# Optimization experiments

Hardware: AMD Instinct MI355X
Metric: run time of the kernel (lower is better)

## Reference

```python
import jax, jax.numpy as jnp
import numpy as np

H = 64
EPS = 1e-5


def _lstm_layer(x, w_ih, w_hh, b_ih, b_hh):
    """Single LSTM layer, batch_first input x: [B, T, I]. PyTorch gate order i,f,g,o."""
    B, T, _ = x.shape
    # precompute input contributions for all timesteps: [B, T, 4H]
    xw = jnp.einsum('bti,gi->btg', x, w_ih) + (b_ih + b_hh)
    xw = jnp.swapaxes(xw, 0, 1)  # [T, B, 4H] for scan over time

    def step(carry, xw_t):
        h, c = carry
        gates = xw_t + h @ w_hh.T  # [B, 4H]
        i, f, g, o = jnp.split(gates, 4, axis=-1)
        i = jax.nn.sigmoid(i)
        f = jax.nn.sigmoid(f)
        g = jnp.tanh(g)
        o = jax.nn.sigmoid(o)
        c = f * c + i * g
        h = o * jnp.tanh(c)
        return (h, c), h

    h0 = jnp.zeros((B, H), x.dtype)
    (_, _), hs = jax.lax.scan(step, (h0, h0), xw)
    return jnp.swapaxes(hs, 0, 1)  # [B, T, H]


def setup_inputs() -> dict:
    key = jax.random.key(0)
    ks = jax.random.split(key, 16)
    B, T, F = 4096, 256, 32
    s = 1.0 / np.sqrt(H)  # PyTorch LSTM init scale
    inp = {
        'x': jax.random.normal(ks[0], (B, T, F), jnp.float32),
        'w_ih0': jax.random.uniform(ks[1], (4 * H, F), jnp.float32, -s, s),
        'w_hh0': jax.random.uniform(ks[2], (4 * H, H), jnp.float32, -s, s),
        'b_ih0': jax.random.uniform(ks[3], (4 * H,), jnp.float32, -s, s),
        'b_hh0': jax.random.uniform(ks[4], (4 * H,), jnp.float32, -s, s),
        'w_ih1': jax.random.uniform(ks[5], (4 * H, H), jnp.float32, -s, s),
        'w_hh1': jax.random.uniform(ks[6], (4 * H, H), jnp.float32, -s, s),
        'b_ih1': jax.random.uniform(ks[7], (4 * H,), jnp.float32, -s, s),
        'b_hh1': jax.random.uniform(ks[8], (4 * H,), jnp.float32, -s, s),
        'ln_g': jnp.ones((H,), jnp.float32),
        'ln_b': jnp.zeros((H,), jnp.float32),
        'w1': jax.random.uniform(ks[9], (64, H), jnp.float32, -s, s),
        'b1': jax.random.uniform(ks[10], (64,), jnp.float32, -s, s),
        'w2': jax.random.uniform(ks[11], (1, 64), jnp.float32, -0.125, 0.125),
        'b2': jax.random.uniform(ks[12], (1,), jnp.float32, -0.125, 0.125),
    }
    return inp


def reference(x, w_ih0, w_hh0, b_ih0, b_hh0, w_ih1, w_hh1, b_ih1, b_hh1,
              ln_g, ln_b, w1, b1, w2, b2):
    out0 = _lstm_layer(x, w_ih0, w_hh0, b_ih0, b_hh0)      # [B, T, H]
    out1 = _lstm_layer(out0, w_ih1, w_hh1, b_ih1, b_hh1)   # [B, T, H]
    last = out1[:, -1, :]                                   # [B, H]
    # LayerNorm
    mu = jnp.mean(last, axis=-1, keepdims=True)
    var = jnp.mean(jnp.square(last - mu), axis=-1, keepdims=True)
    ln = (last - mu) * jax.lax.rsqrt(var + EPS) * ln_g + ln_b
    # MLP head
    h = jax.nn.relu(ln @ w1.T + b1)
    y = h @ w2.T + b2                                       # [B, 1]
    return y[:, 0]
```

## Files before the change

kernel.cpp:

```cpp
#include <hip/hip_runtime.h>

#define TSEQ 256
#define FIN  32
#define HID  64

typedef _Float16 f16x8 __attribute__((ext_vector_type(8)));
typedef float    f32x4 __attribute__((ext_vector_type(4)));

__device__ __forceinline__ float wsum(float v) {
    #pragma unroll
    for (int off = 32; off > 0; off >>= 1) v += __shfl_xor(v, off, 64);
    return v;
}

__device__ __forceinline__ float lstm_cell(const f32x4 g, float& c) {
    float ei = __expf(-g[0]);
    float ef = __expf(-g[1]);
    float yg = __expf(2.0f * g[2]);
    float eo = __expf(-g[3]);
    float sf = __builtin_amdgcn_rcpf(1.0f + ef);
    float ig = (yg - 1.0f) * __builtin_amdgcn_rcpf((1.0f + ei) * (yg + 1.0f));
    c = fmaf(sf, c, ig);
    float cc = fminf(fmaxf(c, -15.0f), 15.0f);
    float yc = __expf(2.0f * cc);
    return (yc - 1.0f) * __builtin_amdgcn_rcpf((1.0f + eo) * (yc + 1.0f));
}

__global__ __launch_bounds__(1024, 4)
void lstm_fused(const float* __restrict__ x,
                const float* __restrict__ w_ih0, const float* __restrict__ w_hh0,
                const float* __restrict__ b_ih0, const float* __restrict__ b_hh0,
                const float* __restrict__ w_ih1, const float* __restrict__ w_hh1,
                const float* __restrict__ b_ih1, const float* __restrict__ b_hh1,
                const float* __restrict__ ln_g, const float* __restrict__ ln_b,
                const float* __restrict__ w1, const float* __restrict__ b1,
                const float* __restrict__ w2, const float* __restrict__ b2,
                float* __restrict__ out)
{
    __shared__ __align__(16) _Float16 X[2][16][32];
    __shared__ __align__(16) _Float16 H0[2][16][72];
    __shared__ __align__(16) _Float16 H1[2][16][72];
    __shared__ __align__(16) float HF[16][68];
    __shared__ __align__(16) float LNB[16][64];

    const int tid  = threadIdx.x;
    const int wave = tid >> 6;
    const int lane = tid & 63;
    const int q    = lane >> 4;
    const int lm   = lane & 15;
    const int q8   = q * 8;
    const int b0   = blockIdx.x * 16;

    const int np   = wave * 16 + lm;
    const int drow = np >> 2;
    const int ty   = np & 3;
    const int row  = ty * 64 + drow;
    const int dq   = wave * 4 + q;

    f16x8 w0f[3], w1f[4];
    f32x4 bias0, bias1;
    {
        const float* p0 = w_ih0 + row * FIN + q8;
        const float* p1 = w_hh0 + row * HID + q8;
        const float* p2 = w_hh0 + row * HID + 32 + q8;
        const float* p3 = w_ih1 + row * HID + q8;
        const float* p4 = w_ih1 + row * HID + 32 + q8;
        const float* p5 = w_hh1 + row * HID + q8;
        const float* p6 = w_hh1 + row * HID + 32 + q8;
        #pragma unroll
        for (int j = 0; j < 8; ++j) {
            w0f[0][j] = (_Float16)p0[j];
            w0f[1][j] = (_Float16)p1[j];
            w0f[2][j] = (_Float16)p2[j];
            w1f[0][j] = (_Float16)p3[j];
            w1f[1][j] = (_Float16)p4[j];
            w1f[2][j] = (_Float16)p5[j];
            w1f[3][j] = (_Float16)p6[j];
        }
        #pragma unroll
        for (int r = 0; r < 4; ++r) {
            bias0[r] = b_ih0[r * 64 + dq] + b_hh0[r * 64 + dq];
            bias1[r] = b_ih1[r * 64 + dq] + b_hh1[r * 64 + dq];
        }
    }

    for (int i = tid; i < 2 * 16 * 72; i += 1024) {
        ((_Float16*)H0)[i] = (_Float16)0.0f;
        ((_Float16*)H1)[i] = (_Float16)0.0f;
    }
    const bool xlane = lane < 32;
    const int  xcol  = lane & 31;
    const float* xbase = x + (size_t)(b0 + wave) * TSEQ * FIN + xcol;
    if (xlane) X[0][wave][xcol] = (_Float16)xbase[0];
    float xw = xbase[FIN];

    float c0 = 0.0f, c1 = 0.0f;
    __syncthreads();

#define INTERVAL(P, DO_A, DO_B, DO_XSTORE, DO_XLOAD, XI)                        \
    {                                                                           \
        float xnew = 0.0f;                                                      \
        if (DO_XLOAD) xnew = xbase[(size_t)(XI) * FIN];                         \
        f16x8 rh0a = *reinterpret_cast<const f16x8*>(&H0[(P) ^ 1][lm][q8]);     \
        f16x8 rh0b = *reinterpret_cast<const f16x8*>(&H0[(P) ^ 1][lm][32 + q8]);\
        if (DO_A) {                                                             \
            f16x8 rx = *reinterpret_cast<const f16x8*>(&X[P][lm][q8]);          \
            f32x4 aA = bias0;                                                   \
            aA = __builtin_amdgcn_mfma_f32_16x16x32_f16(w0f[0], rx,   aA, 0, 0, 0); \
            aA = __builtin_amdgcn_mfma_f32_16x16x32_f16(w0f[1], rh0a, aA, 0, 0, 0); \
            aA = __builtin_amdgcn_mfma_f32_16x16x32_f16(w0f[2], rh0b, aA, 0, 0, 0); \
            float hA = lstm_cell(aA, c0);                                       \
            H0[P][lm][dq] = (_Float16)hA;                                       \
        }                                                                       \
        if (DO_B) {                                                             \
            f16x8 rh1a = *reinterpret_cast<const f16x8*>(&H1[P][lm][q8]);       \
            f16x8 rh1b = *reinterpret_cast<const f16x8*>(&H1[P][lm][32 + q8]);  \
            f32x4 aB = bias1;                                                   \
            aB = __builtin_amdgcn_mfma_f32_16x16x32_f16(w1f[0], rh0a, aB, 0, 0, 0); \
            aB = __builtin_amdgcn_mfma_f32_16x16x32_f16(w1f[1], rh0b, aB, 0, 0, 0); \
            aB = __builtin_amdgcn_mfma_f32_16x16x32_f16(w1f[2], rh1a, aB, 0, 0, 0); \
            aB = __builtin_amdgcn_mfma_f32_16x16x32_f16(w1f[3], rh1b, aB, 0, 0, 0); \
            float hB = lstm_cell(aB, c1);                                       \
            H1[(P) ^ 1][lm][dq] = (_Float16)hB;                                 \
            lastB = hB;                                                         \
        }                                                                       \
        if (DO_XSTORE && xlane) X[(P) ^ 1][wave][xcol] = (_Float16)xw;          \
        xw = xnew;                                                              \
        __syncthreads();                                                        \
    }

    float lastB = 0.0f;

    INTERVAL(0, true, false, true, true, 2)

    #pragma unroll 1
    for (int ii = 0; ii < 127; ++ii) {
        const int i1  = 2 * ii + 1;
        const int xiA = (i1 + 2 > 255) ? 255 : i1 + 2;
        const int xiB = (i1 + 3 > 255) ? 255 : i1 + 3;
        INTERVAL(1, true, true, true, true, xiA)
        INTERVAL(0, true, true, true, true, xiB)
    }

    INTERVAL(1, true, true, false, false, 0)
    INTERVAL(0, false, true, false, false, 0)
    HF[lm][dq] = lastB;
    __syncthreads();

#undef INTERVAL

    const float lngv = ln_g[lane], lnbv = ln_b[lane];
    const float b1v = b1[lane], w2v = w2[lane];
    const float* w1row = w1 + lane * 64;
    {
        float v  = HF[wave][lane];
        float mu = wsum(v) * (1.0f / 64.0f);
        float dv = v - mu;
        float var = wsum(dv * dv) * (1.0f / 64.0f);
        float ln = dv * rsqrtf(var + 1e-5f) * lngv + lnbv;
        LNB[wave][lane] = ln;
        float s = b1v;
        #pragma unroll
        for (int dd = 0; dd < 64; ++dd)
            s = fmaf(LNB[wave][dd], w1row[dd], s);
        s = fmaxf(s, 0.0f);
        float y = wsum(s * w2v);
        if (lane == 0) out[b0 + wave] = y + b2[0];
    }
}

extern "C" void kernel_launch(void* const* d_in, const int* in_sizes, int n_in,
                              void* d_out, int out_size, void* d_ws, size_t ws_size,
                              hipStream_t stream) {
    const float* x     = (const float*)d_in[0];
    const float* w_ih0 = (const float*)d_in[1];
    const float* w_hh0 = (const float*)d_in[2];
    const float* b_ih0 = (const float*)d_in[3];
    const float* b_hh0 = (const float*)d_in[4];
    const float* w_ih1 = (const float*)d_in[5];
    const float* w_hh1 = (const float*)d_in[6];
    const float* b_ih1 = (const float*)d_in[7];
    const float* b_hh1 = (const float*)d_in[8];
    const float* ln_g  = (const float*)d_in[9];
    const float* ln_b  = (const float*)d_in[10];
    const float* w1    = (const float*)d_in[11];
    const float* b1    = (const float*)d_in[12];
    const float* w2    = (const float*)d_in[13];
    const float* b2    = (const float*)d_in[14];
    lstm_fused<<<dim3(256), dim3(1024), 0, stream>>>(
        x, w_ih0, w_hh0, b_ih0, b_hh0,
        w_ih1, w_hh1, b_ih1, b_hh1,
        ln_g, ln_b, w1, b1, w2, b2, (float*)d_out);
}
```

Measured before the change: 372.3 us.

## Specialize waves per LSTM layer and fold exp scaling into weights

Each wave now serves a single LSTM layer: waves 0-7 run layer 0 and waves 8-15 run layer 1. Each wave computes two gate tiles with interleaved independent MFMA chains, so no wave runs both layers' serial MFMA-plus-activation chain in one interval. The -log2e and 2·log2e factors are pre-multiplied into the fp16 weights and biases so the activations use exp2 directly. The x staging through shared memory is also dropped: layer-0 waves load x for the next step straight from global into registers. Trade-offs are possible load imbalance (layer-0 waves do 6 MFMAs, layer-1 waves do 8) and a small fp16 rounding change from the scaled weights.

Result: slower. 420.6 us (+13.0%).

```diff
diff --git a/kernel.cpp b/kernel.cpp
--- a/kernel.cpp
+++ b/kernel.cpp
@@ -3,6 +3,9 @@
 #define TSEQ 256
 #define FIN  32
 #define HID  64
+
+#define LOG2E    1.4426950408889634f
+#define TWOLOG2E 2.8853900817779268f
 
 typedef _Float16 f16x8 __attribute__((ext_vector_type(8)));
 typedef float    f32x4 __attribute__((ext_vector_type(4)));
@@ -14,15 +17,15 @@
 }
 
 __device__ __forceinline__ float lstm_cell(const f32x4 g, float& c) {
-    float ei = __expf(-g[0]);
-    float ef = __expf(-g[1]);
-    float yg = __expf(2.0f * g[2]);
-    float eo = __expf(-g[3]);
+    float ei = __builtin_exp2f(g[0]);
+    float ef = __builtin_exp2f(g[1]);
+    float yg = __builtin_exp2f(g[2]);
+    float eo = __builtin_exp2f(g[3]);
     float sf = __builtin_amdgcn_rcpf(1.0f + ef);
     float ig = (yg - 1.0f) * __builtin_amdgcn_rcpf((1.0f + ei) * (yg + 1.0f));
     c = fmaf(sf, c, ig);
     float cc = fminf(fmaxf(c, -15.0f), 15.0f);
-    float yc = __expf(2.0f * cc);
+    float yc = __builtin_exp2f(TWOLOG2E * cc);
     return (yc - 1.0f) * __builtin_amdgcn_rcpf((1.0f + eo) * (yc + 1.0f));
 }
 
@@ -37,7 +40,6 @@
                 const float* __restrict__ w2, const float* __restrict__ b2,
                 float* __restrict__ out)
 {
-    __shared__ __align__(16) _Float16 X[2][16][32];
     __shared__ __align__(16) _Float16 H0[2][16][72];
     __shared__ __align__(16) _Float16 H1[2][16][72];
     __shared__ __align__(16) float HF[16][68];
@@ -51,103 +53,155 @@
     const int q8   = q * 8;
     const int b0   = blockIdx.x * 16;
 
-    const int np   = wave * 16 + lm;
-    const int drow = np >> 2;
-    const int ty   = np & 3;
-    const int row  = ty * 64 + drow;
-    const int dq   = wave * 4 + q;
-
-    f16x8 w0f[3], w1f[4];
+    const bool isA = wave < 8;
+    const int  wt  = wave & 7;
+    const int  T0  = 2 * wt, T1 = T0 + 1;
+    const int  np0  = T0 * 16 + lm;
+    const int  np1  = T1 * 16 + lm;
+    const int  row0 = (np0 & 3) * 64 + (np0 >> 2);
+    const int  row1 = (np1 & 3) * 64 + (np1 >> 2);
+    const int  d0 = T0 * 4 + q;
+    const int  d1 = T1 * 4 + q;
+    const float wsc = ((lm & 3) == 2) ? TWOLOG2E : -LOG2E;
+
+    f16x8 wf[8];
     f32x4 bias0, bias1;
-    {
-        const float* p0 = w_ih0 + row * FIN + q8;
-        const float* p1 = w_hh0 + row * HID + q8;
-        const float* p2 = w_hh0 + row * HID + 32 + q8;
-        const float* p3 = w_ih1 + row * HID + q8;
-        const float* p4 = w_ih1 + row * HID + 32 + q8;
-        const float* p5 = w_hh1 + row * HID + q8;
-        const float* p6 = w_hh1 + row * HID + 32 + q8;
+    if (isA) {
+        const float* p0 = w_ih0 + row0 * FIN + q8;
+        const float* p1 = w_hh0 + row0 * HID + q8;
+        const float* p2 = w_hh0 + row0 * HID + 32 + q8;
+        const float* p3 = w_ih0 + row1 * FIN + q8;
+        const float* p4 = w_hh0 + row1 * HID + q8;
+        const float* p5 = w_hh0 + row1 * HID + 32 + q8;
         #pragma unroll
         for (int j = 0; j < 8; ++j) {
-            w0f[0][j] = (_Float16)p0[j];
-            w0f[1][j] = (_Float16)p1[j];
-            w0f[2][j] = (_Float16)p2[j];
-            w1f[0][j] = (_Float16)p3[j];
-            w1f[1][j] = (_Float16)p4[j];
-            w1f[2][j] = (_Float16)p5[j];
-            w1f[3][j] = (_Float16)p6[j];
+            wf[0][j] = (_Float16)(wsc * p0[j]);
+            wf[1][j] = (_Float16)(wsc * p1[j]);
+            wf[2][j] = (_Float16)(wsc * p2[j]);
+            wf[3][j] = (_Float16)(wsc * p3[j]);
+            wf[4][j] = (_Float16)(wsc * p4[j]);
+            wf[5][j] = (_Float16)(wsc * p5[j]);
         }
         #pragma unroll
         for (int r = 0; r < 4; ++r) {
-            bias0[r] = b_ih0[r * 64 + dq] + b_hh0[r * 64 + dq];
-            bias1[r] = b_ih1[r * 64 + dq] + b_hh1[r * 64 + dq];
-        }
+            const float s = (r == 2) ? TWOLOG2E : -LOG2E;
+            bias0[r] = s * (b_ih0[r * 64 + d0] + b_hh0[r * 64 + d0]);
+            bias1[r] = s * (b_ih0[r * 64 + d1] + b_hh0[r * 64 + d1]);
+        }
+    } else {
+        const float* p0 = w_ih1 + row0 * HID + q8;
+        const float* p1 = w_ih1 + row0 * HID + 32 + q8;
+        const float* p2 = w_hh1 + row0 * HID + q8;
+        const float* p3 = w_hh1 + row0 * HID + 32 + q8;
+        const float* p4 = w_ih1 + row1 * HID + q8;
+        const float* p5 = w_ih1 + row1 * HID + 32 + q8;
+        const float* p6 = w_hh1 + row1 * HID + q8;
+        const float* p7 = w_hh1 + row1 * HID + 32 + q8;
+        #pragma unroll
+        for (int j = 0; j < 8; ++j) {
+            wf[0][j] = (_Float16)(wsc * p0[j]);
+            wf[1][j] = (_Float16)(wsc * p1[j]);
+            wf[2][j] = (_Float16)(wsc * p2[j]);
+            wf[3][j] = (_Float16)(wsc * p3[j]);
+            wf[4][j] = (_Float16)(wsc * p4[j]);
+            wf[5][j] = (_Float16)(wsc * p5[j]);
+            wf[6][j] = (_Float16)(wsc * p6[j]);
+            wf[7][j] = (_Float16)(wsc * p7[j]);
+        }
+        #pragma unroll
+        for (int r = 0; r < 4; ++r) {
+            const float s = (r == 2) ? TWOLOG2E : -LOG2E;
+            bias0[r] = s * (b_ih1[r * 64 + d0] + b_hh1[r * 64 + d0]);
+            bias1[r] = s * (b_ih1[r * 64 + d1] + b_hh1[r * 64 + d1]);
+        }
+    }
+
+    const float* xp = x + (size_t)(b0 + lm) * TSEQ * FIN + q8;
+    f32x4 xfa, xfb;
+    if (isA) {
+        xfa = *reinterpret_cast<const f32x4*>(xp);
+        xfb = *reinterpret_cast<const f32x4*>(xp + 4);
     }
 
     for (int i = tid; i < 2 * 16 * 72; i += 1024) {
         ((_Float16*)H0)[i] = (_Float16)0.0f;
         ((_Float16*)H1)[i] = (_Float16)0.0f;
     }
-    const bool xlane = lane < 32;
-    const int  xcol  = lane & 31;
-    const float* xbase = x + (size_t)(b0 + wave) * TSEQ * FIN + xcol;
-    if (xlane) X[0][wave][xcol] = (_Float16)xbase[0];
-    float xw = xbase[FIN];
-
-    float c0 = 0.0f, c1 = 0.0f;
+    float c0a = 0.0f, c0b = 0.0f, c1a = 0.0f, c1b = 0.0f;
+    float lastB0 = 0.0f, lastB1 = 0.0f;
     __syncthreads();
 
-#define INTERVAL(P, DO_A, DO_B, DO_XSTORE, DO_XLOAD, XI)                        \
-    {                                                                           \
-        float xnew = 0.0f;                                                      \
-        if (DO_XLOAD) xnew = xbase[(size_t)(XI) * FIN];                         \
-        f16x8 rh0a = *reinterpret_cast<const f16x8*>(&H0[(P) ^ 1][lm][q8]);     \
-        f16x8 rh0b = *reinterpret_cast<const f16x8*>(&H0[(P) ^ 1][lm][32 + q8]);\
-        if (DO_A) {                                                             \
-            f16x8 rx = *reinterpret_cast<const f16x8*>(&X[P][lm][q8]);          \
-            f32x4 aA = bias0;                                                   \
-            aA = __builtin_amdgcn_mfma_f32_16x16x32_f16(w0f[0], rx,   aA, 0, 0, 0); \
-            aA = __builtin_amdgcn_mfma_f32_16x16x32_f16(w0f[1], rh0a, aA, 0, 0, 0); \
-            aA = __builtin_amdgcn_mfma_f32_16x16x32_f16(w0f[2], rh0b, aA, 0, 0, 0); \
-            float hA = lstm_cell(aA, c0);                                       \
-            H0[P][lm][dq] = (_Float16)hA;                                       \
-        }                                                                       \
-        if (DO_B) {                                                             \
-            f16x8 rh1a = *reinterpret_cast<const f16x8*>(&H1[P][lm][q8]);       \
-            f16x8 rh1b = *reinterpret_cast<const f16x8*>(&H1[P][lm][32 + q8]);  \
-            f32x4 aB = bias1;                                                   \
-            aB = __builtin_amdgcn_mfma_f32_16x16x32_f16(w1f[0], rh0a, aB, 0, 0, 0); \
-            aB = __builtin_amdgcn_mfma_f32_16x16x32_f16(w1f[1], rh0b, aB, 0, 0, 0); \
-            aB = __builtin_amdgcn_mfma_f32_16x16x32_f16(w1f[2], rh1a, aB, 0, 0, 0); \
-            aB = __builtin_amdgcn_mfma_f32_16x16x32_f16(w1f[3], rh1b, aB, 0, 0, 0); \
-            float hB = lstm_cell(aB, c1);                                       \
-            H1[(P) ^ 1][lm][dq] = (_Float16)hB;                                 \
-            lastB = hB;                                                         \
-        }                                                                       \
-        if (DO_XSTORE && xlane) X[(P) ^ 1][wave][xcol] = (_Float16)xw;          \
-        xw = xnew;                                                              \
-        __syncthreads();                                                        \
-    }
-
-    float lastB = 0.0f;
-
-    INTERVAL(0, true, false, true, true, 2)
+#define MFMA __builtin_amdgcn_mfma_f32_16x16x32_f16
+#define INTERVAL(P, DO_A, DO_B, DO_XL, XI)                                          \
+    {                                                                               \
+        if (isA) {                                                                  \
+            f16x8 xcur;                                                             \
+            xcur[0] = (_Float16)xfa[0]; xcur[1] = (_Float16)xfa[1];                 \
+            xcur[2] = (_Float16)xfa[2]; xcur[3] = (_Float16)xfa[3];                 \
+            xcur[4] = (_Float16)xfb[0]; xcur[5] = (_Float16)xfb[1];                 \
+            xcur[6] = (_Float16)xfb[2]; xcur[7] = (_Float16)xfb[3];                 \
+            if (DO_XL) {                                                            \
+                xfa = *reinterpret_cast<const f32x4*>(xp + (size_t)(XI) * FIN);     \
+                xfb = *reinterpret_cast<const f32x4*>(xp + (size_t)(XI) * FIN + 4); \
+            }                                                                       \
+            if (DO_A) {                                                             \
+                f16x8 rh0a = *reinterpret_cast<const f16x8*>(&H0[(P) ^ 1][lm][q8]);      \
+                f16x8 rh0b = *reinterpret_cast<const f16x8*>(&H0[(P) ^ 1][lm][32 + q8]); \
+                f32x4 a0 = bias0, a1 = bias1;                                       \
+                a0 = MFMA(wf[0], xcur, a0, 0, 0, 0);                                \
+                a1 = MFMA(wf[3], xcur, a1, 0, 0, 0);                                \
+                a0 = MFMA(wf[1], rh0a, a0, 0, 0, 0);                                \
+                a1 = MFMA(wf[4], rh0a, a1, 0, 0, 0);                                \
+                a0 = MFMA(wf[2], rh0b, a0, 0, 0, 0);                                \
+                a1 = MFMA(wf[5], rh0b, a1, 0, 0, 0);                                \
+                float hv0 = lstm_cell(a0, c0a);                                     \
+                float hv1 = lstm_cell(a1, c0b);                                     \
+                H0[P][lm][d0] = (_Float16)hv0;                                      \
+                H0[P][lm][d1] = (_Float16)hv1;                                      \
+            }                                                                       \
+        } else if (DO_B) {                                                          \
+            f16x8 rh0a = *reinterpret_cast<const f16x8*>(&H0[(P) ^ 1][lm][q8]);      \
+            f16x8 rh0b = *reinterpret_cast<const f16x8*>(&H0[(P) ^ 1][lm][32 + q8]); \
+            f16x8 rh1a = *reinterpret_cast<const f16x8*>(&H1[P][lm][q8]);            \
+            f16x8 rh1b = *reinterpret_cast<const f16x8*>(&H1[P][lm][32 + q8]);       \
+            f32x4 a0 = bias0, a1 = bias1;                                           \
+            a0 = MFMA(wf[0], rh0a, a0, 0, 0, 0);                                    \
+            a1 = MFMA(wf[4], rh0a, a1, 0, 0, 0);                                    \
+            a0 = MFMA(wf[1], rh0b, a0, 0, 0, 0);                                    \
+            a1 = MFMA(wf[5], rh0b, a1, 0, 0, 0);                                    \
+            a0 = MFMA(wf[2], rh1a, a0, 0, 0, 0);                                    \
+            a1 = MFMA(wf[6], rh1a, a1, 0, 0, 0);                                    \
+            a0 = MFMA(wf[3], rh1b, a0, 0, 0, 0);                                    \
+            a1 = MFMA(wf[7], rh1b, a1, 0, 0, 0);                                    \
+            float hv0 = lstm_cell(a0, c1a);                                         \
+            float hv1 = lstm_cell(a1, c1b);                                         \
+            H1[(P) ^ 1][lm][d0] = (_Float16)hv0;                                    \
+            H1[(P) ^ 1][lm][d1] = (_Float16)hv1;                                    \
+            lastB0 = hv0; lastB1 = hv1;                                             \
+        }                                                                           \
+        __syncthreads();                                                            \
+    }
+
+    INTERVAL(0, true, false, true, 1)
 
     #pragma unroll 1
     for (int ii = 0; ii < 127; ++ii) {
-        const int i1  = 2 * ii + 1;
-        const int xiA = (i1 + 2 > 255) ? 255 : i1 + 2;
-        const int xiB = (i1 + 3 > 255) ? 255 : i1 + 3;
-        INTERVAL(1, true, true, true, true, xiA)
-        INTERVAL(0, true, true, true, true, xiB)
-    }
-
-    INTERVAL(1, true, true, false, false, 0)
-    INTERVAL(0, false, true, false, false, 0)
-    HF[lm][dq] = lastB;
+        const int i1 = 2 * ii + 1;
+        INTERVAL(1, true, true, true, i1 + 1)
+        INTERVAL(0, true, true, true, i1 + 2)
+    }
+
+    INTERVAL(1, true, true, false, 0)
+    INTERVAL(0, false, true, false, 0)
+
+#undef INTERVAL
+#undef MFMA
+
+    if (!isA) {
+        HF[lm][d0] = lastB0;
+        HF[lm][d1] = lastB1;
+    }
     __syncthreads();
-
-#undef INTERVAL
 
     const float lngv = ln_g[lane], lnbv = ln_b[lane];
     const float b1v = b1[lane], w2v = w2[lane];
```
